# Kernel optimization log

Measured on AMD Instinct MI355X. Metric: run time of the kernel, lower is better.

The kernel has to match this reference:

```python
import jax, jax.numpy as jnp
import numpy as np

B, S, D_MODEL, H, DK, DV, DOUT = 8, 2048, 1024, 1, 512, 512, 1024
EPS = 1e-6
TEMP = DK ** 0.5


def _ln(x, g, b):
    # LayerNorm over last dim, eps=1e-6, affine
    m = jnp.mean(x, axis=-1, keepdims=True)
    v = jnp.mean((x - m) ** 2, axis=-1, keepdims=True)
    return (x - m) * jax.lax.rsqrt(v + EPS) * g + b


def setup_inputs() -> dict:
    key = jax.random.key(0)
    ks = jax.random.split(key, 16)
    s = 0.02
    return {
        "q": jax.random.normal(ks[0], (B, S, D_MODEL), jnp.float32),
        "k": jax.random.normal(ks[1], (B, S, D_MODEL), jnp.float32),
        "v": jax.random.normal(ks[2], (B, S, D_MODEL), jnp.float32),
        "mask": jnp.ones((B, S, S), jnp.int32),
        "Wq": jax.random.normal(ks[3], (D_MODEL, H * DK), jnp.float32) * s,
        "bq": jnp.zeros((H * DK,), jnp.float32),
        "Wk": jax.random.normal(ks[4], (D_MODEL, H * DK), jnp.float32) * s,
        "bk": jnp.zeros((H * DK,), jnp.float32),
        "Wv": jax.random.normal(ks[5], (D_MODEL, H * DV), jnp.float32) * s,
        "bv": jnp.zeros((H * DV,), jnp.float32),
        "g_q": jnp.ones((H * DK,), jnp.float32),
        "be_q": jnp.zeros((H * DK,), jnp.float32),
        "g_k": jnp.ones((H * DK,), jnp.float32),
        "be_k": jnp.zeros((H * DK,), jnp.float32),
        "g_v": jnp.ones((H * DV,), jnp.float32),
        "be_v": jnp.zeros((H * DV,), jnp.float32),
        "W1": jax.random.normal(ks[6], (H * DV, H * DV), jnp.float32) * s,
        "b1": jnp.zeros((H * DV,), jnp.float32),
        "W2": jax.random.normal(ks[7], (H * DV, DOUT), jnp.float32) * s,
        "b2": jnp.zeros((DOUT,), jnp.float32),
    }


def reference(q, k, v, mask, Wq, bq, Wk, bk, Wv, bv, g_q, be_q, g_k, be_k, g_v, be_v, W1, b1, W2, b2):
    # QKV projections, viewed as (B, S, H, d)
    qp = (q @ Wq + bq).reshape(B, S, H, DK)
    kp = (k @ Wk + bk).reshape(B, S, H, DK)
    vp = (v @ Wv + bv).reshape(B, S, H, DV)
    residual = qp
    # per-(token,head) LayerNorm over last dim (valid only because H == 1 in source)
    qn = jnp.swapaxes(_ln(qp, g_q, be_q), 1, 2)  # (B, H, S, DK)
    kn = jnp.swapaxes(_ln(kp, g_k, be_k), 1, 2)
    vn = jnp.swapaxes(_ln(vp, g_v, be_v), 1, 2)
    # scaled dot-product attention with mask
    scores = jnp.einsum('bhqd,bhkd->bhqk', qn / TEMP, kn)
    scores = jnp.where(mask[:, None, :, :] == 0, -1e9, scores)
    attn = jax.nn.softmax(scores, axis=-1)
    out = jnp.einsum('bhqk,bhkd->bhqd', attn, vn)
    out = jnp.swapaxes(out, 1, 2).reshape(B, S, H * DV)
    # trailing 2-layer MLP
    out = jax.nn.relu(out @ W1 + b1) @ W2 + b2
    return (out, residual, jnp.squeeze(attn))
```

## Files before the change

kernel.cpp:

```cpp
#include <hip/hip_runtime.h>
#include <hip/hip_bf16.h>

typedef __attribute__((ext_vector_type(8))) short short8;
typedef __attribute__((ext_vector_type(4))) short short4v;
typedef __attribute__((ext_vector_type(4))) float f32x4;

#define INV_TEMP 0.044194173824159216f

__device__ __forceinline__ ushort f2bf(float f) {
  unsigned u = __float_as_uint(f);
  unsigned r = (u + 0x7FFFu + ((u >> 16) & 1u)) >> 16;
  return (ushort)r;
}
__device__ __forceinline__ float bf2f(ushort u) {
  union { unsigned i; float f; } x; x.i = ((unsigned)u) << 16; return x.f;
}

__device__ __forceinline__ void gload_lds16(const void* g, void* l) {
  __builtin_amdgcn_global_load_lds(
      (const __attribute__((address_space(1))) unsigned int*)(unsigned long long)(uintptr_t)g,
      (__attribute__((address_space(3))) unsigned int*)(unsigned)(uintptr_t)l,
      16, 0, 0);
}

__global__ __launch_bounds__(256)
void transpose_cvt_all(const float* __restrict__ Wq, const float* __restrict__ Wk,
                       const float* __restrict__ Wv, const float* __restrict__ W1,
                       const float* __restrict__ W2,
                       ushort* __restrict__ Tq, ushort* __restrict__ Tk,
                       ushort* __restrict__ Tv, ushort* __restrict__ T1,
                       ushort* __restrict__ T2) {
  const int z = blockIdx.z;
  const int K = (z < 3) ? 1024 : 512;
  const int N = (z == 4) ? 1024 : 512;
  if (blockIdx.x * 32 >= N || blockIdx.y * 32 >= K) return;
  const float* W = z == 0 ? Wq : (z == 1 ? Wk : (z == 2 ? Wv : (z == 3 ? W1 : W2)));
  ushort* WT = z == 0 ? Tq : (z == 1 ? Tk : (z == 2 ? Tv : (z == 3 ? T1 : T2)));
  __shared__ float tile[32][33];
  const int n0 = blockIdx.x * 32, k0 = blockIdx.y * 32;
  const int tx = threadIdx.x & 31, ty = threadIdx.x >> 5;
  #pragma unroll
  for (int i = ty; i < 32; i += 8)
    tile[i][tx] = W[(long)(k0 + i) * N + n0 + tx];
  __syncthreads();
  #pragma unroll
  for (int i = ty; i < 32; i += 8)
    WT[(long)(n0 + i) * K + k0 + tx] = f2bf(tile[tx][i]);
}

__global__ __launch_bounds__(256)
void transpose_bf16(const ushort* __restrict__ in, ushort* __restrict__ out, int S, int D) {
  __shared__ ushort tile[32][33];
  const ushort* inb = in + (long)blockIdx.z * S * D;
  ushort* outb = out + (long)blockIdx.z * S * D;
  const int d0 = blockIdx.x * 32, s0 = blockIdx.y * 32;
  const int tx = threadIdx.x & 31, ty = threadIdx.x >> 5;
  #pragma unroll
  for (int i = ty; i < 32; i += 8)
    tile[i][tx] = inb[(long)(s0 + i) * D + d0 + tx];
  __syncthreads();
  #pragma unroll
  for (int i = ty; i < 32; i += 8)
    outb[(long)(d0 + i) * S + s0 + tx] = tile[tx][i];
}

__global__ __launch_bounds__(256)
void ln3_kernel(const float* __restrict__ Xq, const ushort* __restrict__ Xk,
                const ushort* __restrict__ Xv,
                const float* __restrict__ gq, const float* __restrict__ beq,
                const float* __restrict__ gk, const float* __restrict__ bek,
                const float* __restrict__ gv, const float* __restrict__ bev,
                ushort* __restrict__ Oq, ushort* __restrict__ Ok, ushort* __restrict__ Ov) {
  const int which = blockIdx.y;
  const float* g = which == 0 ? gq : (which == 1 ? gk : gv);
  const float* be = which == 0 ? beq : (which == 1 ? bek : bev);
  ushort* out = which == 0 ? Oq : (which == 1 ? Ok : Ov);
  const float scale = which == 0 ? INV_TEMP : 1.0f;

  const int row = blockIdx.x * 4 + (threadIdx.x >> 6);
  const int lane = threadIdx.x & 63;
  f32x4 v0, v1;
  if (which == 0) {
    const float* x = Xq + (long)row * 512 + lane * 8;
    v0 = *(const f32x4*)x;
    v1 = *(const f32x4*)(x + 4);
  } else {
    const ushort* x = (which == 1 ? Xk : Xv) + (long)row * 512 + lane * 8;
    short8 vv = *(const short8*)x;
    #pragma unroll
    for (int j = 0; j < 4; j++) { v0[j] = bf2f((ushort)vv[j]); v1[j] = bf2f((ushort)vv[4 + j]); }
  }
  float s = v0[0]+v0[1]+v0[2]+v0[3]+v1[0]+v1[1]+v1[2]+v1[3];
  float ss = v0[0]*v0[0]+v0[1]*v0[1]+v0[2]*v0[2]+v0[3]*v0[3]
           + v1[0]*v1[0]+v1[1]*v1[1]+v1[2]*v1[2]+v1[3]*v1[3];
  #pragma unroll
  for (int off = 32; off; off >>= 1) { s += __shfl_xor(s, off); ss += __shfl_xor(ss, off); }
  const float mean = s * (1.0f/512.0f);
  const float var  = ss * (1.0f/512.0f) - mean*mean;
  const float rs = rsqrtf(var + 1e-6f);
  f32x4 g0 = *(const f32x4*)(g + lane*8);
  f32x4 g1 = *(const f32x4*)(g + lane*8 + 4);
  f32x4 b0 = *(const f32x4*)(be + lane*8);
  f32x4 b1 = *(const f32x4*)(be + lane*8 + 4);
  union { short8 v; ushort u[8]; } o;
  #pragma unroll
  for (int j = 0; j < 4; j++) o.u[j]     = f2bf(((v0[j]-mean)*rs*g0[j] + b0[j]) * scale);
  #pragma unroll
  for (int j = 0; j < 4; j++) o.u[4 + j] = f2bf(((v1[j]-mean)*rs*g1[j] + b1[j]) * scale);
  *(short8*)(out + (long)row * 512 + lane * 8) = o.v;
}

__global__ __launch_bounds__(512)
void gemm_scores256(const ushort* __restrict__ qn, const ushort* __restrict__ kn,
                    const int* __restrict__ maskp, ushort* __restrict__ Cb,
                    float* __restrict__ partial) {
  __shared__ char smem_raw[131072];
  ushort (*As)[16384] = (ushort(*)[16384])smem_raw;
  ushort (*Bs)[16384] = (ushort(*)[16384])(smem_raw + 65536);
  float* smf = (float*)smem_raw;

  const int tid = threadIdx.x;
  const int lane = tid & 63;
  const int wave = tid >> 6;
  const int wr = wave >> 2;
  const int wc = wave & 3;

  int lin = blockIdx.x + 8 * (blockIdx.y + 8 * blockIdx.z);
  const int q8 = 64;
  const int swz = (lin & 7) * q8 + (lin >> 3);
  const int bx = swz & 7;
  const int by = (swz >> 3) & 7;
  const int bz = swz >> 6;

  const long zb = bz;
  const ushort* Ab = qn + zb * (2048L * 512) + (long)by * 256 * 512;
  const ushort* Bb = kn + zb * (2048L * 512) + (long)bx * 256 * 512;
  const int nt = 8;

  auto stage = [&](int buf, int t) {
    const long kt = (long)t << 6;
    #pragma unroll
    for (int i = 0; i < 4; i++) {
      const int c = i * 512 + tid;
      const int row = c >> 3, g = c & 7, gsrc = g ^ (row & 7);
      gload_lds16(Ab + (long)row * 512 + kt + gsrc * 8, (char*)As[buf] + c * 16);
      gload_lds16(Bb + (long)row * 512 + kt + gsrc * 8, (char*)Bs[buf] + c * 16);
    }
  };

  f32x4 acc[8][4];
  #pragma unroll
  for (int m = 0; m < 8; m++)
    #pragma unroll
    for (int n = 0; n < 4; n++)
      acc[m][n] = f32x4{0.f, 0.f, 0.f, 0.f};

  stage(0, 0);
  stage(1, 1);

  for (int t = 0; t < nt; ++t) {
    const int buf = t & 1;
    if (t == nt - 1) {
      asm volatile("s_waitcnt vmcnt(0)" ::: "memory");
    } else {
      asm volatile("s_waitcnt vmcnt(8)" ::: "memory");
    }
    __builtin_amdgcn_s_barrier();
    __builtin_amdgcn_sched_barrier(0);

    #pragma unroll
    for (int ks = 0; ks < 2; ks++) {
      short8 af[8], bfr[4];
      const int kb = ks * 64 + ((lane >> 4) << 4);
      #pragma unroll
      for (int m = 0; m < 8; m++) {
        const int row = wr * 128 + m * 16 + (lane & 15);
        af[m] = *(const short8*)((const char*)As[buf] +
                 ((row << 7) | (kb ^ ((row & 7) << 4))));
      }
      #pragma unroll
      for (int n = 0; n < 4; n++) {
        const int col = wc * 64 + n * 16 + (lane & 15);
        bfr[n] = *(const short8*)((const char*)Bs[buf] +
                  ((col << 7) | (kb ^ ((col & 7) << 4))));
      }
      __builtin_amdgcn_s_setprio(1);
      #pragma unroll
      for (int m = 0; m < 8; m++)
        #pragma unroll
        for (int n = 0; n < 4; n++)
          acc[m][n] = __builtin_amdgcn_mfma_f32_16x16x32_bf16(af[m], bfr[n], acc[m][n], 0, 0, 0);
      __builtin_amdgcn_s_setprio(0);
    }
    __builtin_amdgcn_sched_barrier(0);
    __builtin_amdgcn_s_barrier();
    __builtin_amdgcn_sched_barrier(0);
    if (t + 2 < nt) stage(buf, t + 2);
  }

  const int c_lane = lane & 15;
  const int r_lane = (lane >> 4) << 2;
  const int r_own = tid >> 3;
  const int cq = (tid & 7) * 32;
  #pragma unroll
  for (int p = 0; p < 4; p++) {
    const int grow = by * 256 + p * 64 + r_own;
    const int gcol = bx * 256 + cq;
    const int* mrow = maskp + zb * 4194304L + (long)grow * 2048 + gcol;
    int4 mk[8];
    #pragma unroll
    for (int cc = 0; cc < 8; cc++) mk[cc] = *(const int4*)(mrow + cc * 4);

    __syncthreads();
    if (wr == (p >> 1)) {
      const int mbase = (p & 1) * 4;
      #pragma unroll
      for (int mm = 0; mm < 4; mm++)
        #pragma unroll
        for (int n = 0; n < 4; n++)
          #pragma unroll
          for (int r4 = 0; r4 < 4; r4++)
            smf[(mm * 16 + r_lane + r4) * 260 + wc * 64 + n * 16 + c_lane] =
                acc[mbase + mm][n][r4];
    }
    __syncthreads();

    ushort* orow = Cb + zb * 4194304L + (long)grow * 2048 + gcol;
    float rsum = 0.f;
    #pragma unroll
    for (int cc = 0; cc < 4; cc++) {
      f32x4 v0 = *(const f32x4*)&smf[r_own * 260 + cq + cc * 8];
      f32x4 v1 = *(const f32x4*)&smf[r_own * 260 + cq + cc * 8 + 4];
      int4 m0 = mk[cc * 2], m1 = mk[cc * 2 + 1];
      float e0 = m0.x ? __expf(v0[0]) : 0.f;
      float e1 = m0.y ? __expf(v0[1]) : 0.f;
      float e2 = m0.z ? __expf(v0[2]) : 0.f;
      float e3 = m0.w ? __expf(v0[3]) : 0.f;
      float e4 = m1.x ? __expf(v1[0]) : 0.f;
      float e5 = m1.y ? __expf(v1[1]) : 0.f;
      float e6 = m1.z ? __expf(v1[2]) : 0.f;
      float e7 = m1.w ? __expf(v1[3]) : 0.f;
      rsum += (e0 + e1 + e2 + e3) + (e4 + e5 + e6 + e7);
      union { short8 s; ushort u[8]; } o;
      o.u[0] = f2bf(e0); o.u[1] = f2bf(e1); o.u[2] = f2bf(e2); o.u[3] = f2bf(e3);
      o.u[4] = f2bf(e4); o.u[5] = f2bf(e5); o.u[6] = f2bf(e6); o.u[7] = f2bf(e7);
      *(short8*)(orow + cc * 8) = o.s;
    }
    rsum += __shfl_xor(rsum, 1);
    rsum += __shfl_xor(rsum, 2);
    rsum += __shfl_xor(rsum, 4);
    if ((tid & 7) == 0)
      partial[((long)zb * 8 + bx) * 2048 + grow] = rsum;
  }
}

template<int EPI, bool HAS_BIAS, bool OUT_BF16, bool A_F32>
__global__ __launch_bounds__(256)
void gemm_tn_pipe(const void* __restrict__ Av, const ushort* __restrict__ Bt,
                  const float* __restrict__ bias,
                  float* __restrict__ Cf, ushort* __restrict__ Cb,
                  float* __restrict__ partial,
                  const float* __restrict__ A2, const float* __restrict__ A3,
                  const ushort* __restrict__ Bt2, const ushort* __restrict__ Bt3,
                  const float* __restrict__ bias2, const float* __restrict__ bias3,
                  ushort* __restrict__ Cb2,
                  int M, int N, int K,
                  long sA, long sB, long sC) {
  __shared__ char smem_raw[66048];
  ushort (*As)[128 * 64] = (ushort(*)[128 * 64])smem_raw;
  ushort (*Bs)[128 * 64] = (ushort(*)[128 * 64])(smem_raw + 32768);
  float* zloc = (float*)(smem_raw + 65536);

  const int tid = threadIdx.x;
  const int lane = tid & 63;
  const int wave = tid >> 6;
  const int wr = wave >> 1;
  const int wc = wave & 1;

  const int gx = gridDim.x, gy = gridDim.y;
  int lin = blockIdx.x + gx * (blockIdx.y + gy * blockIdx.z);
  const int nwg = gx * gy * (int)gridDim.z;
  int swz = lin;
  if ((nwg & 7) == 0) {
    const int q8 = nwg >> 3;
    swz = (lin & 7) * q8 + (lin >> 3);
  }
  const int bx = swz % gx;
  const int tmp = swz / gx;
  const int by = tmp % gy;
  const int bz = tmp / gy;

  const long zb = bz;
  const float* Afp;
  const ushort* Bb;
  const float* bias_p = bias;
  if constexpr (EPI == 4) {
    Afp = (bz == 0 ? (const float*)Av : (bz == 1 ? A2 : A3)) + (long)by * 128 * K;
    Bb = (bz == 0 ? Bt : (bz == 1 ? Bt2 : Bt3)) + (long)bx * 128 * K;
    bias_p = bz == 0 ? bias : (bz == 1 ? bias2 : bias3);
  } else {
    Afp = (const float*)Av + zb * sA + (long)by * 128 * K;
    Bb = Bt + zb * sB + (long)bx * 128 * K;
  }
  const ushort* Ab = (const ushort*)Av + zb * sA + (long)by * 128 * K;
  const int rowbase0 = by * 128;
  const int nt = K >> 6;

  if constexpr (EPI == 3) {
    if (tid < 128) {
      float z = 0.f;
      #pragma unroll
      for (int j = 0; j < 8; j++)
        z += partial[((long)(zb * 8 + j)) * 2048 + rowbase0 + tid];
      zloc[tid] = 1.0f / z;
    }
  }

  auto stage = [&](int buf, int t) {
    const long kt = (long)t << 6;
    if constexpr (A_F32) {
      f32x4 a[4][2];
      #pragma unroll
      for (int i = 0; i < 4; i++) {
        const int c = i * 256 + tid;
        const int row = c >> 3, g = c & 7;
        const float* p = Afp + (long)row * K + kt + g * 8;
        a[i][0] = *(const f32x4*)p;
        a[i][1] = *(const f32x4*)(p + 4);
      }
      #pragma unroll
      for (int i = 0; i < 4; i++) {
        const int c = i * 256 + tid;
        const int row = c >> 3, g = c & 7, gsrc = g ^ (row & 7);
        gload_lds16(Bb + (long)row * K + kt + gsrc * 8, (char*)Bs[buf] + c * 16);
      }
      #pragma unroll
      for (int i = 0; i < 4; i++) {
        const int c = i * 256 + tid;
        const int row = c >> 3, g = c & 7;
        union { short8 s; ushort u[8]; } o;
        #pragma unroll
        for (int j = 0; j < 4; j++) { o.u[j] = f2bf(a[i][0][j]); o.u[4 + j] = f2bf(a[i][1][j]); }
        *(short8*)((char*)As[buf] + ((row << 7) | ((g << 4) ^ ((row & 7) << 4)))) = o.s;
      }
      asm volatile("s_waitcnt lgkmcnt(0)" ::: "memory");
    } else {
      #pragma unroll
      for (int i = 0; i < 4; i++) {
        const int c = i * 256 + tid;
        const int row = c >> 3, g = c & 7, gsrc = g ^ (row & 7);
        gload_lds16(Ab + (long)row * K + kt + gsrc * 8, (char*)As[buf] + c * 16);
        gload_lds16(Bb + (long)row * K + kt + gsrc * 8, (char*)Bs[buf] + c * 16);
      }
    }
  };

  f32x4 acc[4][4];
  #pragma unroll
  for (int m = 0; m < 4; m++)
    #pragma unroll
    for (int n = 0; n < 4; n++)
      acc[m][n] = f32x4{0.f, 0.f, 0.f, 0.f};

  stage(0, 0);
  stage(1, 1);

  for (int t = 0; t < nt; ++t) {
    const int buf = t & 1;
    if (t == nt - 1) {
      asm volatile("s_waitcnt vmcnt(0)" ::: "memory");
    } else if constexpr (A_F32) {
      asm volatile("s_waitcnt vmcnt(4)" ::: "memory");
    } else {
      asm volatile("s_waitcnt vmcnt(8)" ::: "memory");
    }
    __builtin_amdgcn_s_barrier();
    __builtin_amdgcn_sched_barrier(0);

    if constexpr (EPI == 3) {
      if ((t >> 3) == bx) {
        #pragma unroll
        for (int e = 0; e < 4; e++) {
          const int c = e * 256 + tid;
          const int row = c >> 3, g = c & 7;
          short8 p8 = *(const short8*)((const char*)As[buf] +
                       ((row << 7) | ((g ^ (row & 7)) << 4)));
          const float iz = zloc[row];
          f32x4 o0, o1;
          #pragma unroll
          for (int jj = 0; jj < 4; jj++) {
            o0[jj] = bf2f((ushort)p8[jj]) * iz;
            o1[jj] = bf2f((ushort)p8[4 + jj]) * iz;
          }
          float* dst = Cf + zb * 4194304L + (long)(rowbase0 + row) * 2048 + (t << 6) + g * 8;
          *(f32x4*)dst = o0;
          *(f32x4*)(dst + 4) = o1;
        }
      }
    }

    #pragma unroll
    for (int ks = 0; ks < 2; ks++) {
      short8 af[4], bfr[4];
      const int kb = ks * 64 + ((lane >> 4) << 4);
      #pragma unroll
      for (int m = 0; m < 4; m++) {
        const int row = wr * 64 + m * 16 + (lane & 15);
        af[m] = *(const short8*)((const char*)As[buf] +
                 ((row << 7) | (kb ^ ((row & 7) << 4))));
      }
      #pragma unroll
      for (int n = 0; n < 4; n++) {
        const int col = wc * 64 + n * 16 + (lane & 15);
        bfr[n] = *(const short8*)((const char*)Bs[buf] +
                  ((col << 7) | (kb ^ ((col & 7) << 4))));
      }
      __builtin_amdgcn_s_setprio(1);
      #pragma unroll
      for (int m = 0; m < 4; m++)
        #pragma unroll
        for (int n = 0; n < 4; n++)
          acc[m][n] = __builtin_amdgcn_mfma_f32_16x16x32_bf16(af[m], bfr[n], acc[m][n], 0, 0, 0);
      __builtin_amdgcn_s_setprio(0);
    }
    __builtin_amdgcn_sched_barrier(0);
    __builtin_amdgcn_s_barrier();
    __builtin_amdgcn_sched_barrier(0);
    if (t + 2 < nt) stage(buf, t + 2);
  }

  const int c_lane = lane & 15;
  const int r_lane = (lane >> 4) << 2;
  const int colbase = bx * 128 + wc * 64;
  const int rowbase = by * 128 + wr * 64;
  #pragma unroll
  for (int n = 0; n < 4; n++) {
    const int col = colbase + n * 16 + c_lane;
    const float bv = HAS_BIAS ? bias_p[col] : 0.0f;
    #pragma unroll
    for (int m = 0; m < 4; m++) {
      const int rbase = rowbase + m * 16 + r_lane;
      #pragma unroll
      for (int r4 = 0; r4 < 4; r4++) {
        const int row = rbase + r4;
        float vv = acc[m][n][r4] + bv;
        if constexpr (EPI == 1) vv = fmaxf(vv, 0.0f);
        if constexpr (EPI == 3) vv *= zloc[wr * 64 + m * 16 + r_lane + r4];
        const long off = zb * sC + (long)row * N + col;
        if constexpr (EPI == 4) {
          if (bz == 0) Cf[off] = vv;
          else if (bz == 1) Cb[off] = f2bf(vv);
          else Cb2[off] = f2bf(vv);
        } else if constexpr (OUT_BF16) {
          Cb[off] = f2bf(vv);
        } else {
          Cf[off] = vv;
        }
      }
    }
  }
}

extern "C" void kernel_launch(void* const* d_in, const int* in_sizes, int n_in,
                              void* d_out, int out_size, void* d_ws, size_t ws_size,
                              hipStream_t stream) {
  const float* q    = (const float*)d_in[0];
  const float* k    = (const float*)d_in[1];
  const float* v    = (const float*)d_in[2];
  const int*   mask = (const int*)d_in[3];
  const float* Wq   = (const float*)d_in[4];
  const float* bq   = (const float*)d_in[5];
  const float* Wk   = (const float*)d_in[6];
  const float* bk   = (const float*)d_in[7];
  const float* Wv   = (const float*)d_in[8];
  const float* bv   = (const float*)d_in[9];
  const float* g_q  = (const float*)d_in[10];
  const float* be_q = (const float*)d_in[11];
  const float* g_k  = (const float*)d_in[12];
  const float* be_k = (const float*)d_in[13];
  const float* g_v  = (const float*)d_in[14];
  const float* be_v = (const float*)d_in[15];
  const float* W1   = (const float*)d_in[16];
  const float* b1   = (const float*)d_in[17];
  const float* W2   = (const float*)d_in[18];
  const float* b2   = (const float*)d_in[19];

  float* out_mlp  = (float*)d_out;
  float* out_res  = out_mlp + 16777216L;
  float* out_attn = out_res + 8388608L;

  char* w = (char*)d_ws;
  ushort* qn      = (ushort*)(w);
  ushort* kn      = (ushort*)(w + 16777216UL);
  ushort* kp_bf   = (ushort*)(w + 33554432UL);
  ushort* vp_bf   = (ushort*)(w + 50331648UL);
  ushort* attn_bf = (ushort*)(w + 33554432UL);
  ushort* vn      = (ushort*)(w + 100663296UL);
  ushort* vnT     = (ushort*)(w + 117440512UL);
  ushort* pv      = (ushort*)(w + 134217728UL);
  ushort* h       = (ushort*)(w + 150994944UL);
  ushort* wqT     = (ushort*)(w + 167772160UL);
  ushort* wkT     = (ushort*)(w + 168820736UL);
  ushort* wvT     = (ushort*)(w + 169869312UL);
  ushort* w1T     = (ushort*)(w + 170917888UL);
  ushort* w2T     = (ushort*)(w + 171442176UL);
  float*  partial = (float*)(w + 172490752UL);

  dim3 blk(256);

  transpose_cvt_all<<<dim3(32, 32, 5), blk, 0, stream>>>(
      Wq, Wk, Wv, W1, W2, wqT, wkT, wvT, w1T, w2T);

  gemm_tn_pipe<4, true, false, true><<<dim3(4, 128, 3), blk, 0, stream>>>(
      q, wqT, bq, out_res, kp_bf, nullptr,
      k, v, wkT, wvT, bk, bv, vp_bf,
      16384, 512, 1024, 0, 0, 0);

  ln3_kernel<<<dim3(4096, 3), blk, 0, stream>>>(
      out_res, kp_bf, vp_bf, g_q, be_q, g_k, be_k, g_v, be_v, qn, kn, vn);

  transpose_bf16<<<dim3(16, 64, 8), blk, 0, stream>>>(vn, vnT, 2048, 512);

  gemm_scores256<<<dim3(8, 8, 8), dim3(512), 0, stream>>>(
      qn, kn, mask, attn_bf, partial);

  gemm_tn_pipe<3, false, true, false><<<dim3(4, 16, 8), blk, 0, stream>>>(
      attn_bf, vnT, nullptr, out_attn, pv, partial,
      nullptr, nullptr, nullptr, nullptr, nullptr, nullptr, nullptr,
      2048, 512, 2048,
      (long)2048 * 2048, (long)512 * 2048, (long)2048 * 512);

  gemm_tn_pipe<1, true, true, false><<<dim3(4, 128, 1), blk, 0, stream>>>(
      pv, w1T, b1, nullptr, h, nullptr,
      nullptr, nullptr, nullptr, nullptr, nullptr, nullptr, nullptr,
      16384, 512, 512, 0, 0, 0);
  gemm_tn_pipe<0, true, false, false><<<dim3(8, 128, 1), blk, 0, stream>>>(
      h, w2T, b2, out_mlp, nullptr, nullptr,
      nullptr, nullptr, nullptr, nullptr, nullptr, nullptr, nullptr,
      16384, 1024, 512, 0, 0, 0);
}
```

Before: 355.7 us.

## Add dedicated software-pipelined QKV projection GEMM with register-staged fp32 A loads

Replaces the generic templated fp32-A path of the QKV projection with a dedicated kernel. The new kernel prefetches the next fp32 A tile into registers while MFMAs run on the current LDS buffer, and only converts and writes it to LDS after the compute phase. B tiles keep using direct global-to-LDS loads. Scheduling barriers and s_setprio control instruction ordering. The aim is to hide fp32 load latency and the conversion cost, in exchange for holding two register sets for A, which raises register pressure.

```diff
diff --git a/kernel.cpp b/kernel.cpp
--- a/kernel.cpp
+++ b/kernel.cpp
@@ -108,6 +108,169 @@
   #pragma unroll
   for (int j = 0; j < 4; j++) o.u[4 + j] = f2bf(((v1[j]-mean)*rs*g1[j] + b1[j]) * scale);
   *(short8*)(out + (long)row * 512 + lane * 8) = o.v;
+}
+
+__global__ __launch_bounds__(256)
+void gemm_proj(const float* __restrict__ Aq, const float* __restrict__ Ak,
+               const float* __restrict__ Avv,
+               const ushort* __restrict__ Bq, const ushort* __restrict__ Bk,
+               const ushort* __restrict__ Bv,
+               const float* __restrict__ bq, const float* __restrict__ bk,
+               const float* __restrict__ bv,
+               float* __restrict__ Oq, ushort* __restrict__ Ok,
+               ushort* __restrict__ Ov) {
+  constexpr int K = 1024;
+  __shared__ char smem_raw[65536];
+  ushort (*As)[8192] = (ushort(*)[8192])smem_raw;
+  ushort (*Bs)[8192] = (ushort(*)[8192])(smem_raw + 32768);
+
+  const int tid = threadIdx.x;
+  const int lane = tid & 63;
+  const int wave = tid >> 6;
+  const int wr = wave >> 1;
+  const int wc = wave & 1;
+
+  int lin = blockIdx.x + 4 * (blockIdx.y + 128 * blockIdx.z);
+  const int q8 = 192;
+  const int swz = (lin & 7) * q8 + (lin >> 3);
+  const int bx = swz & 3;
+  const int by = (swz >> 2) & 127;
+  const int bz = swz >> 9;
+
+  const float* Afp = (bz == 0 ? Aq : (bz == 1 ? Ak : Avv)) + (long)by * 128 * K;
+  const ushort* Bb = (bz == 0 ? Bq : (bz == 1 ? Bk : Bv)) + (long)bx * 128 * K;
+  const float* bias_p = bz == 0 ? bq : (bz == 1 ? bk : bv);
+
+  auto loadA = [&](int t, f32x4 (&a)[4][2]) {
+    const long kt = (long)t << 6;
+    #pragma unroll
+    for (int i = 0; i < 4; i++) {
+      const int c = i * 256 + tid;
+      const int row = c >> 3, g = c & 7;
+      const float* p = Afp + (long)row * K + kt + g * 8;
+      a[i][0] = *(const f32x4*)p;
+      a[i][1] = *(const f32x4*)(p + 4);
+    }
+  };
+  auto writeA = [&](int buf, const f32x4 (&a)[4][2]) {
+    #pragma unroll
+    for (int i = 0; i < 4; i++) {
+      const int c = i * 256 + tid;
+      const int row = c >> 3, g = c & 7;
+      union { short8 s; ushort u[8]; } o;
+      #pragma unroll
+      for (int j = 0; j < 4; j++) { o.u[j] = f2bf(a[i][0][j]); o.u[4 + j] = f2bf(a[i][1][j]); }
+      *(short8*)((char*)As[buf] + ((row << 7) | ((g << 4) ^ ((row & 7) << 4)))) = o.s;
+    }
+    asm volatile("s_waitcnt lgkmcnt(0)" ::: "memory");
+  };
+  auto stageB = [&](int buf, int t) {
+    const long kt = (long)t << 6;
+    #pragma unroll
+    for (int i = 0; i < 4; i++) {
+      const int c = i * 256 + tid;
+      const int row = c >> 3, g = c & 7, gsrc = g ^ (row & 7);
+      gload_lds16(Bb + (long)row * K + kt + gsrc * 8, (char*)Bs[buf] + c * 16);
+    }
+  };
+
+  f32x4 acc[4][4];
+  #pragma unroll
+  for (int m = 0; m < 4; m++)
+    #pragma unroll
+    for (int n = 0; n < 4; n++)
+      acc[m][n] = f32x4{0.f, 0.f, 0.f, 0.f};
+
+  f32x4 aE[4][2], aO[4][2];
+
+  loadA(0, aE);
+  writeA(0, aE);
+  __builtin_amdgcn_sched_barrier(0);
+  stageB(0, 0);
+  __builtin_amdgcn_sched_barrier(0);
+  loadA(1, aO);
+  __builtin_amdgcn_sched_barrier(0);
+  stageB(1, 1);
+  __builtin_amdgcn_sched_barrier(0);
+
+  auto mfma_phase = [&](int buf) {
+    #pragma unroll
+    for (int ks = 0; ks < 2; ks++) {
+      short8 af[4], bfr[4];
+      const int kb = ks * 64 + ((lane >> 4) << 4);
+      #pragma unroll
+      for (int m = 0; m < 4; m++) {
+        const int row = wr * 64 + m * 16 + (lane & 15);
+        af[m] = *(const short8*)((const char*)As[buf] +
+                 ((row << 7) | (kb ^ ((row & 7) << 4))));
+      }
+      #pragma unroll
+      for (int n = 0; n < 4; n++) {
+        const int col = wc * 64 + n * 16 + (lane & 15);
+        bfr[n] = *(const short8*)((const char*)Bs[buf] +
+                  ((col << 7) | (kb ^ ((col & 7) << 4))));
+      }
+      __builtin_amdgcn_s_setprio(1);
+      #pragma unroll
+      for (int m = 0; m < 4; m++)
+        #pragma unroll
+        for (int n = 0; n < 4; n++)
+          acc[m][n] = __builtin_amdgcn_mfma_f32_16x16x32_bf16(af[m], bfr[n], acc[m][n], 0, 0, 0);
+      __builtin_amdgcn_s_setprio(0);
+    }
+  };
+
+  #pragma unroll 1
+  for (int tt = 0; tt < 8; ++tt) {
+    const bool lastp = (tt == 7);
+    asm volatile("s_waitcnt vmcnt(12)" ::: "memory");
+    __builtin_amdgcn_s_barrier();
+    __builtin_amdgcn_sched_barrier(0);
+    mfma_phase(0);
+    __builtin_amdgcn_sched_barrier(0);
+    __builtin_amdgcn_s_barrier();
+    __builtin_amdgcn_sched_barrier(0);
+    writeA(1, aO);
+    if (!lastp) { loadA(2 * tt + 2, aE); stageB(0, 2 * tt + 2); }
+    __builtin_amdgcn_sched_barrier(0);
+    if (lastp) asm volatile("s_waitcnt vmcnt(0)" ::: "memory");
+    else       asm volatile("s_waitcnt vmcnt(12)" ::: "memory");
+    __builtin_amdgcn_s_barrier();
+    __builtin_amdgcn_sched_barrier(0);
+    mfma_phase(1);
+    __builtin_amdgcn_sched_barrier(0);
+    __builtin_amdgcn_s_barrier();
+    __builtin_amdgcn_sched_barrier(0);
+    if (!lastp) {
+      writeA(0, aE);
+      loadA(2 * tt + 3, aO);
+      stageB(1, 2 * tt + 3);
+    }
+    __builtin_amdgcn_sched_barrier(0);
+  }
+
+  const int c_lane = lane & 15;
+  const int r_lane = (lane >> 4) << 2;
+  const int colbase = bx * 128 + wc * 64;
+  const int rowbase = by * 128 + wr * 64;
+  #pragma unroll
+  for (int n = 0; n < 4; n++) {
+    const int col = colbase + n * 16 + c_lane;
+    const float bv2 = bias_p[col];
+    #pragma unroll
+    for (int m = 0; m < 4; m++) {
+      const int rbase = rowbase + m * 16 + r_lane;
+      #pragma unroll
+      for (int r4 = 0; r4 < 4; r4++) {
+        const int row = rbase + r4;
+        const float vv = acc[m][n][r4] + bv2;
+        const long off = (long)row * 512 + col;
+        if (bz == 0)      Oq[off] = vv;
+        else if (bz == 1) Ok[off] = f2bf(vv);
+        else              Ov[off] = f2bf(vv);
+      }
+    }
+  }
 }
 
 __global__ __launch_bounds__(512)
@@ -254,16 +417,12 @@
   }
 }
 
-template<int EPI, bool HAS_BIAS, bool OUT_BF16, bool A_F32>
+template<int EPI, bool HAS_BIAS, bool OUT_BF16>
 __global__ __launch_bounds__(256)
-void gemm_tn_pipe(const void* __restrict__ Av, const ushort* __restrict__ Bt,
+void gemm_tn_pipe(const ushort* __restrict__ Ain, const ushort* __restrict__ Bt,
                   const float* __restrict__ bias,
                   float* __restrict__ Cf, ushort* __restrict__ Cb,
                   float* __restrict__ partial,
-                  const float* __restrict__ A2, const float* __restrict__ A3,
-                  const ushort* __restrict__ Bt2, const ushort* __restrict__ Bt3,
-                  const float* __restrict__ bias2, const float* __restrict__ bias3,
-                  ushort* __restrict__ Cb2,
                   int M, int N, int K,
                   long sA, long sB, long sC) {
   __shared__ char smem_raw[66048];
@@ -291,18 +450,8 @@
   const int bz = tmp / gy;
 
   const long zb = bz;
-  const float* Afp;
-  const ushort* Bb;
-  const float* bias_p = bias;
-  if constexpr (EPI == 4) {
-    Afp = (bz == 0 ? (const float*)Av : (bz == 1 ? A2 : A3)) + (long)by * 128 * K;
-    Bb = (bz == 0 ? Bt : (bz == 1 ? Bt2 : Bt3)) + (long)bx * 128 * K;
-    bias_p = bz == 0 ? bias : (bz == 1 ? bias2 : bias3);
-  } else {
-    Afp = (const float*)Av + zb * sA + (long)by * 128 * K;
-    Bb = Bt + zb * sB + (long)bx * 128 * K;
-  }
-  const ushort* Ab = (const ushort*)Av + zb * sA + (long)by * 128 * K;
+  const ushort* Ab = Ain + zb * sA + (long)by * 128 * K;
+  const ushort* Bb = Bt + zb * sB + (long)bx * 128 * K;
   const int rowbase0 = by * 128;
   const int nt = K >> 6;
 
@@ -318,40 +467,12 @@
 
   auto stage = [&](int buf, int t) {
     const long kt = (long)t << 6;
-    if constexpr (A_F32) {
-      f32x4 a[4][2];
-      #pragma unroll
-      for (int i = 0; i < 4; i++) {
-        const int c = i * 256 + tid;
-        const int row = c >> 3, g = c & 7;
-        const float* p = Afp + (long)row * K + kt + g * 8;
-        a[i][0] = *(const f32x4*)p;
-        a[i][1] = *(const f32x4*)(p + 4);
-      }
-      #pragma unroll
-      for (int i = 0; i < 4; i++) {
-        const int c = i * 256 + tid;
-        const int row = c >> 3, g = c & 7, gsrc = g ^ (row & 7);
-        gload_lds16(Bb + (long)row * K + kt + gsrc * 8, (char*)Bs[buf] + c * 16);
-      }
-      #pragma unroll
-      for (int i = 0; i < 4; i++) {
-        const int c = i * 256 + tid;
-        const int row = c >> 3, g = c & 7;
-        union { short8 s; ushort u[8]; } o;
-        #pragma unroll
-        for (int j = 0; j < 4; j++) { o.u[j] = f2bf(a[i][0][j]); o.u[4 + j] = f2bf(a[i][1][j]); }
-        *(short8*)((char*)As[buf] + ((row << 7) | ((g << 4) ^ ((row & 7) << 4)))) = o.s;
-      }
-      asm volatile("s_waitcnt lgkmcnt(0)" ::: "memory");
-    } else {
-      #pragma unroll
-      for (int i = 0; i < 4; i++) {
-        const int c = i * 256 + tid;
-        const int row = c >> 3, g = c & 7, gsrc = g ^ (row & 7);
-        gload_lds16(Ab + (long)row * K + kt + gsrc * 8, (char*)As[buf] + c * 16);
-        gload_lds16(Bb + (long)row * K + kt + gsrc * 8, (char*)Bs[buf] + c * 16);
-      }
+    #pragma unroll
+    for (int i = 0; i < 4; i++) {
+      const int c = i * 256 + tid;
+      const int row = c >> 3, g = c & 7, gsrc = g ^ (row & 7);
+      gload_lds16(Ab + (long)row * K + kt + gsrc * 8, (char*)As[buf] + c * 16);
+      gload_lds16(Bb + (long)row * K + kt + gsrc * 8, (char*)Bs[buf] + c * 16);
     }
   };
 
@@ -369,8 +490,6 @@
     const int buf = t & 1;
     if (t == nt - 1) {
       asm volatile("s_waitcnt vmcnt(0)" ::: "memory");
-    } else if constexpr (A_F32) {
-      asm volatile("s_waitcnt vmcnt(4)" ::: "memory");
     } else {
       asm volatile("s_waitcnt vmcnt(8)" ::: "memory");
     }
@@ -436,7 +555,7 @@
   #pragma unroll
   for (int n = 0; n < 4; n++) {
     const int col = colbase + n * 16 + c_lane;
-    const float bv = HAS_BIAS ? bias_p[col] : 0.0f;
+    const float bv = HAS_BIAS ? bias[col] : 0.0f;
     #pragma unroll
     for (int m = 0; m < 4; m++) {
       const int rbase = rowbase + m * 16 + r_lane;
@@ -447,15 +566,8 @@
         if constexpr (EPI == 1) vv = fmaxf(vv, 0.0f);
         if constexpr (EPI == 3) vv *= zloc[wr * 64 + m * 16 + r_lane + r4];
         const long off = zb * sC + (long)row * N + col;
-        if constexpr (EPI == 4) {
-          if (bz == 0) Cf[off] = vv;
-          else if (bz == 1) Cb[off] = f2bf(vv);
-          else Cb2[off] = f2bf(vv);
-        } else if constexpr (OUT_BF16) {
-          Cb[off] = f2bf(vv);
-        } else {
-          Cf[off] = vv;
-        }
+        if constexpr (OUT_BF16) Cb[off] = f2bf(vv);
+        else                    Cf[off] = vv;
       }
     }
   }
@@ -511,10 +623,8 @@
   transpose_cvt_all<<<dim3(32, 32, 5), blk, 0, stream>>>(
       Wq, Wk, Wv, W1, W2, wqT, wkT, wvT, w1T, w2T);
 
-  gemm_tn_pipe<4, true, false, true><<<dim3(4, 128, 3), blk, 0, stream>>>(
-      q, wqT, bq, out_res, kp_bf, nullptr,
-      k, v, wkT, wvT, bk, bv, vp_bf,
-      16384, 512, 1024, 0, 0, 0);
+  gemm_proj<<<dim3(4, 128, 3), blk, 0, stream>>>(
+      q, k, v, wqT, wkT, wvT, bq, bk, bv, out_res, kp_bf, vp_bf);
 
   ln3_kernel<<<dim3(4096, 3), blk, 0, stream>>>(
       out_res, kp_bf, vp_bf, g_q, be_q, g_k, be_k, g_v, be_v, qn, kn, vn);
@@ -524,18 +634,15 @@
   gemm_scores256<<<dim3(8, 8, 8), dim3(512), 0, stream>>>(
       qn, kn, mask, attn_bf, partial);
 
-  gemm_tn_pipe<3, false, true, false><<<dim3(4, 16, 8), blk, 0, stream>>>(
+  gemm_tn_pipe<3, false, true><<<dim3(4, 16, 8), blk, 0, stream>>>(
       attn_bf, vnT, nullptr, out_attn, pv, partial,
-      nullptr, nullptr, nullptr, nullptr, nullptr, nullptr, nullptr,
       2048, 512, 2048,
       (long)2048 * 2048, (long)512 * 2048, (long)2048 * 512);
 
-  gemm_tn_pipe<1, true, true, false><<<dim3(4, 128, 1), blk, 0, stream>>>(
+  gemm_tn_pipe<1, true, true><<<dim3(4, 128, 1), blk, 0, stream>>>(
       pv, w1T, b1, nullptr, h, nullptr,
-      nullptr, nullptr, nullptr, nullptr, nullptr, nullptr, nullptr,
       16384, 512, 512, 0, 0, 0);
-  gemm_tn_pipe<0, true, false, false><<<dim3(8, 128, 1), blk, 0, stream>>>(
+  gemm_tn_pipe<0, true, false><<<dim3(8, 128, 1), blk, 0, stream>>>(
       h, w2T, b2, out_mlp, nullptr, nullptr,
-      nullptr, nullptr, nullptr, nullptr, nullptr, nullptr, nullptr,
       16384, 1024, 512, 0, 0, 0);
 }
```

New measurement: 343.1 us, median of 2. 1.04x faster.
